# Optimization experiments

Hardware: AMD Instinct MI355X
Metric: run time of the kernel (lower is better)

Reference implementation:

```python
import jax, jax.numpy as jnp
import numpy as np
import math

HEADS = 16
D_MODEL = 1024
D_K = D_MODEL // HEADS


def setup_inputs() -> dict:
    key = jax.random.key(0)
    ks = jax.random.split(key, 11)
    B, S = 2, 2048
    s = 1.0 / math.sqrt(D_MODEL)
    return {
        "q": jax.random.normal(ks[0], (B, S, D_MODEL), jnp.float32),
        "k": jax.random.normal(ks[1], (B, S, D_MODEL), jnp.float32),
        "v": jax.random.normal(ks[2], (B, S, D_MODEL), jnp.float32),
        "Wq": jax.random.normal(ks[3], (D_MODEL, D_MODEL), jnp.float32) * s,
        "bq": jax.random.normal(ks[4], (D_MODEL,), jnp.float32) * s,
        "Wk": jax.random.normal(ks[5], (D_MODEL, D_MODEL), jnp.float32) * s,
        "bk": jax.random.normal(ks[6], (D_MODEL,), jnp.float32) * s,
        "Wv": jax.random.normal(ks[7], (D_MODEL, D_MODEL), jnp.float32) * s,
        "bv": jax.random.normal(ks[8], (D_MODEL,), jnp.float32) * s,
        "Wo": jax.random.normal(ks[9], (D_MODEL, D_MODEL), jnp.float32) * s,
        "bo": jax.random.normal(ks[10], (D_MODEL,), jnp.float32) * s,
    }


def reference(q, k, v, Wq, bq, Wk, bk, Wv, bv, Wo, bo):
    B, S, _ = q.shape
    # linear projections, split heads: [B, H, S, d_k]
    def proj(x, W, b):
        y = x @ W.T + b
        return y.reshape(B, -1, HEADS, D_K).transpose(0, 2, 1, 3)
    qh, kh, vh = proj(q, Wq, bq), proj(k, Wk, bk), proj(v, Wv, bv)
    # abs-modified scaled dot-product attention (no mask, eval -> no dropout)
    scores = jnp.abs(jnp.einsum("bhsd,bhtd->bhst", qh, kh) / math.sqrt(D_K))
    attn = jax.nn.softmax(scores, axis=-1)
    out = jnp.einsum("bhst,bhtd->bhsd", attn, vh)
    concat = out.transpose(0, 2, 1, 3).reshape(B, S, D_MODEL)
    return concat @ Wo.T + bo
```

## Files before the change

kernel.cpp:

```cpp
#include <hip/hip_runtime.h>
#include <hip/hip_bf16.h>

#define HEADS 16
#define DK 64
#define DM 1024
#define SEQ 2048
#define BATCH 2

using bf16x8 = __attribute__((ext_vector_type(8))) short;
using short4v = __attribute__((ext_vector_type(4))) short;
using f32x4 = __attribute__((ext_vector_type(4))) float;

static __device__ __forceinline__ short f2bf(float x) {
  union { float f; unsigned u; } c;
  c.f = x;
  unsigned r = (c.u + 0x7FFFu + ((c.u >> 16) & 1u)) >> 16;
  return (short)r;
}

static __device__ __forceinline__ unsigned pk2bf(float lo, float hi) {
  union { __hip_bfloat162 h; unsigned u; } c;
  c.h = __float22bfloat162_rn(float2{lo, hi});
  return c.u;
}

static __device__ __forceinline__ void gload_lds16(const void* g, void* l) {
  __builtin_amdgcn_global_load_lds(
      (const __attribute__((address_space(1))) void*)g,
      (__attribute__((address_space(3))) void*)l, 16, 0, 0);
}

__global__ __launch_bounds__(256) void cvt7(
    const float* __restrict__ s0, const float* __restrict__ s1,
    const float* __restrict__ s2, const float* __restrict__ s3,
    const float* __restrict__ s4, const float* __restrict__ s5,
    const float* __restrict__ s6, short* d0, short* d1, short* d2, short* d3,
    short* d4, short* d5, short* d6) {
  const int y = blockIdx.y;
  const float* s;
  short* d;
  int n;
  switch (y) {
    case 0: s = s0; d = d0; n = BATCH * SEQ * DM; break;
    case 1: s = s1; d = d1; n = BATCH * SEQ * DM; break;
    case 2: s = s2; d = d2; n = BATCH * SEQ * DM; break;
    case 3: s = s3; d = d3; n = DM * DM; break;
    case 4: s = s4; d = d4; n = DM * DM; break;
    case 5: s = s5; d = d5; n = DM * DM; break;
    default: s = s6; d = d6; n = DM * DM; break;
  }
  const int n4 = n >> 2;
  const int stride = gridDim.x * 256;
  for (int i = blockIdx.x * 256 + threadIdx.x; i < n4; i += stride) {
    float4 v = ((const float4*)s)[i];
    short4v o;
    o.x = f2bf(v.x);
    o.y = f2bf(v.y);
    o.z = f2bf(v.z);
    o.w = f2bf(v.w);
    ((short4v*)d)[i] = o;
  }
}

__global__ __launch_bounds__(256) void proj_qkv(
    const short* __restrict__ Aq, const short* __restrict__ Ak,
    const short* __restrict__ Av, const short* __restrict__ Wq_,
    const short* __restrict__ Wk_, const short* __restrict__ Wv_,
    const float* __restrict__ bq, const float* __restrict__ bk,
    const float* __restrict__ bv, short* __restrict__ Qh,
    short* __restrict__ Kh, short* __restrict__ Vt) {
  __shared__ short smem[128 * 136];
  short* As = smem;
  short* Ws = smem + 8192;

  const int z = blockIdx.z;
  const short* A = z == 0 ? Aq : z == 1 ? Ak : Av;
  const short* W = z == 0 ? Wq_ : z == 1 ? Wk_ : Wv_;
  const float* bias = z == 0 ? bq : z == 1 ? bk : bv;
  short* C = z == 0 ? Qh : z == 1 ? Kh : Vt;
  const bool tr = (z == 2);

  const int tid = threadIdx.x;
  const int wave = tid >> 6, lane = tid & 63;
  const int quad = lane >> 4, l15 = lane & 15;
  const int n0 = blockIdx.x * 128, m0 = blockIdx.y * 128;
  const int mh = (wave & 1) * 64, nh = (wave >> 1) * 64;
  const int ldr = lane >> 3, ldc = lane & 7;

  f32x4 acc[4][4] = {};

  for (int k0 = 0; k0 < 1024; k0 += 64) {
    __syncthreads();
#pragma unroll
    for (int i = 0; i < 8; ++i) {
      int seg = wave * 8 + i;
      int r = (seg & 15) * 8 + ldr;
      int kb = ldc ^ (r & 7);
      if (seg < 16)
        gload_lds16(&A[(size_t)(m0 + r) * 1024 + k0 + kb * 8], &As[seg * 512]);
      else
        gload_lds16(&W[(size_t)(n0 + r) * 1024 + k0 + kb * 8],
                    &Ws[(seg - 16) * 512]);
    }
    __syncthreads();
#pragma unroll
    for (int ks = 0; ks < 2; ++ks) {
      bf16x8 a[4], b[4];
      int kb = ks * 4 + quad;
#pragma unroll
      for (int f = 0; f < 4; ++f) {
        int rm = mh + f * 16 + l15;
        int rn = nh + f * 16 + l15;
        a[f] = *(const bf16x8*)&As[rm * 64 + (kb ^ (rm & 7)) * 8];
        b[f] = *(const bf16x8*)&Ws[rn * 64 + (kb ^ (rn & 7)) * 8];
      }
#pragma unroll
      for (int mf = 0; mf < 4; ++mf)
#pragma unroll
        for (int nf = 0; nf < 4; ++nf)
          acc[mf][nf] = __builtin_amdgcn_mfma_f32_16x16x32_bf16(
              a[mf], b[nf], acc[mf][nf], 0, 0, 0);
    }
  }

  float bvv[4];
#pragma unroll
  for (int nf = 0; nf < 4; ++nf) bvv[nf] = bias[n0 + nh + nf * 16 + l15];

  __syncthreads();
  short* Cb = smem;

  if (!tr) {
    const float osc = (z == 0) ? 0.18033688011112042f : 1.0f;
#pragma unroll
    for (int mf = 0; mf < 4; ++mf)
#pragma unroll
      for (int nf = 0; nf < 4; ++nf)
#pragma unroll
        for (int r = 0; r < 4; ++r)
          Cb[(mh + mf * 16 + quad * 4 + r) * 136 + nh + nf * 16 + l15] =
              f2bf((acc[mf][nf][r] + bvv[nf]) * osc);
    __syncthreads();
#pragma unroll
    for (int j = 0; j < 8; ++j) {
      int cid = tid + 256 * j;
      int row = cid >> 4, cb = cid & 15;
      bf16x8 v = *(const bf16x8*)&Cb[row * 136 + cb * 8];
      int m = m0 + row, n = n0 + cb * 8;
      int b = m >> 11, s = m & (SEQ - 1), h = n >> 6, d = n & 63;
      *(bf16x8*)&C[((size_t)(b * HEADS + h) * SEQ + s) * DK + d] = v;
    }
  } else {
#pragma unroll
    for (int mf = 0; mf < 4; ++mf)
#pragma unroll
      for (int nf = 0; nf < 4; ++nf) {
        short4v p;
        p.x = f2bf(acc[mf][nf][0] + bvv[nf]);
        p.y = f2bf(acc[mf][nf][1] + bvv[nf]);
        p.z = f2bf(acc[mf][nf][2] + bvv[nf]);
        p.w = f2bf(acc[mf][nf][3] + bvv[nf]);
        *(short4v*)&Cb[(nh + nf * 16 + l15) * 136 + mh + mf * 16 + quad * 4] =
            p;
      }
    __syncthreads();
#pragma unroll
    for (int j = 0; j < 8; ++j) {
      int cid = tid + 256 * j;
      int row = cid >> 4, cb = cid & 15;
      bf16x8 v = *(const bf16x8*)&Cb[row * 136 + cb * 8];
      int n = n0 + row, m = m0 + cb * 8;
      int b = m >> 11, s = m & (SEQ - 1), h = n >> 6, d = n & 63;
      *(bf16x8*)&C[((size_t)(b * HEADS + h) * DK + d) * SEQ + s] = v;
    }
  }
}

__global__ __launch_bounds__(256) void proj_out(const short* __restrict__ A,
                                                const short* __restrict__ W,
                                                const float* __restrict__ bias,
                                                float* __restrict__ C) {
  __shared__ short smem[128 * 136];
  short* As = smem;
  short* Ws = smem + 8192;

  const int tid = threadIdx.x;
  const int wave = tid >> 6, lane = tid & 63;
  const int quad = lane >> 4, l15 = lane & 15;
  const int n0 = blockIdx.x * 128, m0 = blockIdx.y * 128;
  const int mh = (wave & 1) * 64, nh = (wave >> 1) * 64;
  const int ldr = lane >> 3, ldc = lane & 7;

  f32x4 acc[4][4] = {};

  for (int k0 = 0; k0 < 1024; k0 += 64) {
    __syncthreads();
#pragma unroll
    for (int i = 0; i < 8; ++i) {
      int seg = wave * 8 + i;
      int r = (seg & 15) * 8 + ldr;
      int kb = ldc ^ (r & 7);
      if (seg < 16)
        gload_lds16(&A[(size_t)(m0 + r) * 1024 + k0 + kb * 8], &As[seg * 512]);
      else
        gload_lds16(&W[(size_t)(n0 + r) * 1024 + k0 + kb * 8],
                    &Ws[(seg - 16) * 512]);
    }
    __syncthreads();
#pragma unroll
    for (int ks = 0; ks < 2; ++ks) {
      bf16x8 a[4], b[4];
      int kb = ks * 4 + quad;
#pragma unroll
      for (int f = 0; f < 4; ++f) {
        int rm = mh + f * 16 + l15;
        int rn = nh + f * 16 + l15;
        a[f] = *(const bf16x8*)&As[rm * 64 + (kb ^ (rm & 7)) * 8];
        b[f] = *(const bf16x8*)&Ws[rn * 64 + (kb ^ (rn & 7)) * 8];
      }
#pragma unroll
      for (int mf = 0; mf < 4; ++mf)
#pragma unroll
        for (int nf = 0; nf < 4; ++nf)
          acc[mf][nf] = __builtin_amdgcn_mfma_f32_16x16x32_bf16(
              a[mf], b[nf], acc[mf][nf], 0, 0, 0);
    }
  }

  float bvv[4];
#pragma unroll
  for (int nf = 0; nf < 4; ++nf) bvv[nf] = bias[n0 + nh + nf * 16 + l15];
#pragma unroll
  for (int mf = 0; mf < 4; ++mf)
#pragma unroll
    for (int nf = 0; nf < 4; ++nf)
#pragma unroll
      for (int r = 0; r < 4; ++r)
        C[(size_t)(m0 + mh + mf * 16 + quad * 4 + r) * 1024 + n0 + nh +
          nf * 16 + l15] = acc[mf][nf][r] + bvv[nf];
}

__global__ __launch_bounds__(256) void attn_mfma(const short* __restrict__ Qh,
                                                 const short* __restrict__ Kh,
                                                 const short* __restrict__ VtG,
                                                 short* __restrict__ concat) {
  __shared__ short Ksm[2][64 * 64];
  __shared__ short Vsm[2][64 * 64];

  const int tid = threadIdx.x;
  const int wave = tid >> 6, lane = tid & 63;
  const int quad = lane >> 4, l15 = lane & 15;
  const int bh = blockIdx.y;
  const int q0 = blockIdx.x * 128;
  const size_t base = (size_t)bh * SEQ * DK;
  const int ldr = lane >> 3, ldc = lane & 7;
  const int NT = SEQ / 64;

  bf16x8 qf[2][2];
#pragma unroll
  for (int mf = 0; mf < 2; ++mf)
#pragma unroll
    for (int ks = 0; ks < 2; ++ks)
      qf[mf][ks] =
          *(const bf16x8*)&Qh[base +
                              (size_t)(q0 + wave * 32 + mf * 16 + l15) * 64 +
                              ks * 32 + quad * 8];

  bf16x8 ones;
#pragma unroll
  for (int i = 0; i < 8; ++i) ones[i] = (short)0x3F80;

  f32x4 O[2][4] = {};
  f32x4 Lacc[2] = {};

  int krow[4];
#pragma unroll
  for (int kf = 0; kf < 4; ++kf)
    krow[kf] = 32 * (kf >> 1) + 8 * (l15 >> 2) + 4 * (kf & 1) + (l15 & 3);

  auto stage = [&](int kt, int buf) {
#pragma unroll
    for (int i = 0; i < 2; ++i) {
      int seg = wave * 2 + i;
      int r = seg * 8 + ldr;
      int kswz = (r & 7) ^ (((r >> 3) & 3) << 1);
      gload_lds16(&Kh[base + (size_t)(kt * 64 + r) * 64 + (ldc ^ kswz) * 8],
                  &Ksm[buf][seg * 512]);
      gload_lds16(&VtG[base + (size_t)r * SEQ + kt * 64 + (ldc ^ (r & 7)) * 8],
                  &Vsm[buf][seg * 512]);
    }
  };

  stage(0, 0);
  __syncthreads();

  int cur = 0;
  for (int kt = 0; kt < NT; ++kt) {
    if (kt + 1 < NT) stage(kt + 1, cur ^ 1);

    const short* Ks = Ksm[cur];
    const short* Vs = Vsm[cur];

    f32x4 sf[2][4] = {};
#pragma unroll
    for (int ks = 0; ks < 2; ++ks) {
      bf16x8 kfr[4];
      int kb = ks * 4 + quad;
#pragma unroll
      for (int kf = 0; kf < 4; ++kf) {
        int n = krow[kf];
        int kswz = (n & 7) ^ (((n >> 3) & 3) << 1);
        kfr[kf] = *(const bf16x8*)&Ks[n * 64 + ((kb ^ kswz) << 3)];
      }
      __builtin_amdgcn_s_setprio(1);
#pragma unroll
      for (int kf = 0; kf < 4; ++kf)
#pragma unroll
        for (int mf = 0; mf < 2; ++mf)
          sf[mf][kf] = __builtin_amdgcn_mfma_f32_16x16x32_bf16(
              kfr[kf], qf[mf][ks], sf[mf][kf], 0, 0, 0);
      __builtin_amdgcn_s_setprio(0);
    }

    bf16x8 pa[2][2];
#pragma unroll
    for (int mf = 0; mf < 2; ++mf)
#pragma unroll
      for (int ks = 0; ks < 2; ++ks) {
        float e[8];
#pragma unroll
        for (int half = 0; half < 2; ++half)
#pragma unroll
          for (int r = 0; r < 4; ++r)
            e[half * 4 + r] =
                __builtin_amdgcn_exp2f(fabsf(sf[mf][2 * ks + half][r]));
        union { unsigned u[4]; bf16x8 v; } t;
        t.u[0] = pk2bf(e[0], e[1]);
        t.u[1] = pk2bf(e[2], e[3]);
        t.u[2] = pk2bf(e[4], e[5]);
        t.u[3] = pk2bf(e[6], e[7]);
        pa[mf][ks] = t.v;
      }

#pragma unroll
    for (int ks = 0; ks < 2; ++ks) {
      int kb = ks * 4 + quad;
      bf16x8 bvf[4];
#pragma unroll
      for (int nf = 0; nf < 4; ++nf) {
        int d = nf * 16 + l15;
        bvf[nf] = *(const bf16x8*)&Vs[d * 64 + ((kb ^ (d & 7)) << 3)];
      }
      __builtin_amdgcn_s_setprio(1);
#pragma unroll
      for (int mf = 0; mf < 2; ++mf) {
#pragma unroll
        for (int nf = 0; nf < 4; ++nf)
          O[mf][nf] = __builtin_amdgcn_mfma_f32_16x16x32_bf16(
              pa[mf][ks], bvf[nf], O[mf][nf], 0, 0, 0);
        Lacc[mf] = __builtin_amdgcn_mfma_f32_16x16x32_bf16(pa[mf][ks], ones,
                                                           Lacc[mf], 0, 0, 0);
      }
      __builtin_amdgcn_s_setprio(0);
    }

    __syncthreads();
    cur ^= 1;
  }

  float inv_[2][4];
#pragma unroll
  for (int mf = 0; mf < 2; ++mf)
#pragma unroll
    for (int r = 0; r < 4; ++r) inv_[mf][r] = 1.f / Lacc[mf][r];

  short* Es = (short*)Ksm;
#pragma unroll
  for (int mf = 0; mf < 2; ++mf)
#pragma unroll
    for (int nf = 0; nf < 4; ++nf)
#pragma unroll
      for (int r = 0; r < 4; ++r) {
        int rw = wave * 32 + mf * 16 + quad * 4 + r;
        int d = nf * 16 + l15;
        Es[rw * 64 + (((d >> 3) ^ (rw & 7)) << 3) + (d & 7)] =
            f2bf(O[mf][nf][r] * inv_[mf][r]);
      }
  __syncthreads();
  const int b = bh >> 4, h = bh & 15;
#pragma unroll
  for (int j = 0; j < 4; ++j) {
    int cid = tid + 256 * j;
    int rw = cid >> 3, g = cid & 7;
    bf16x8 v = *(const bf16x8*)&Es[rw * 64 + ((g ^ (rw & 7)) << 3)];
    *(bf16x8*)&concat[((size_t)(b * SEQ + q0 + rw)) * DM + h * 64 + g * 8] = v;
  }
}

extern "C" void kernel_launch(void* const* d_in, const int* in_sizes, int n_in,
                              void* d_out, int out_size, void* d_ws,
                              size_t ws_size, hipStream_t stream) {
  const float* q = (const float*)d_in[0];
  const float* k = (const float*)d_in[1];
  const float* v = (const float*)d_in[2];
  const float* Wq = (const float*)d_in[3];
  const float* bq = (const float*)d_in[4];
  const float* Wk = (const float*)d_in[5];
  const float* bk = (const float*)d_in[6];
  const float* Wv = (const float*)d_in[7];
  const float* bv = (const float*)d_in[8];
  const float* Wo = (const float*)d_in[9];
  const float* bo = (const float*)d_in[10];

  short* ws = (short*)d_ws;
  const size_t T4 = (size_t)BATCH * SEQ * DM;
  const size_t T1 = (size_t)DM * DM;
  short* qb = ws;
  short* kb_ = ws + T4;
  short* vb = ws + 2 * T4;
  short* Wqb = ws + 3 * T4;
  short* Wkb = Wqb + T1;
  short* Wvb = Wqb + 2 * T1;
  short* Wob = Wqb + 3 * T1;
  short* Qh = Wqb + 4 * T1;
  short* Kh = Qh + T4;
  short* VtG = Qh + 2 * T4;
  short* cc = Qh + 3 * T4;

  cvt7<<<dim3(1024, 7), 256, 0, stream>>>(q, k, v, Wq, Wk, Wv, Wo, qb, kb_, vb,
                                          Wqb, Wkb, Wvb, Wob);

  proj_qkv<<<dim3(DM / 128, (BATCH * SEQ) / 128, 3), 256, 0, stream>>>(
      qb, kb_, vb, Wqb, Wkb, Wvb, bq, bk, bv, Qh, Kh, VtG);

  attn_mfma<<<dim3(SEQ / 128, BATCH * HEADS), 256, 0, stream>>>(Qh, Kh, VtG,
                                                                cc);

  proj_out<<<dim3(DM / 128, (BATCH * SEQ) / 128), 256, 0, stream>>>(
      cc, Wob, bo, (float*)d_out);
}
```

Before: 237.5 us.

## Split attention key tiles across two wave groups with LDS reduction

Doubles the attention block to 512 threads. Two groups of four waves each handle half of every 64-key tile for the same 128 query rows, and their partial O and row-sum accumulators are combined through shared memory at the end. The goal is more waves per block for latency hiding, with half the per-wave work in the inner loop. The cost is a final LDS reduction with extra barriers, duplicated Q fragments across the two groups, and lower per-wave MFMA density.

```diff
diff --git a/kernel.cpp b/kernel.cpp
--- a/kernel.cpp
+++ b/kernel.cpp
@@ -240,16 +240,19 @@
           nf * 16 + l15] = acc[mf][nf][r] + bvv[nf];
 }
 
-__global__ __launch_bounds__(256) void attn_mfma(const short* __restrict__ Qh,
-                                                 const short* __restrict__ Kh,
-                                                 const short* __restrict__ VtG,
-                                                 short* __restrict__ concat) {
-  __shared__ short Ksm[2][64 * 64];
-  __shared__ short Vsm[2][64 * 64];
+__global__ __launch_bounds__(512, 4) void attn_mfma(
+    const short* __restrict__ Qh, const short* __restrict__ Kh,
+    const short* __restrict__ VtG, short* __restrict__ concat) {
+  __shared__ __align__(16) short smem[4 * 64 * 64];
+  __shared__ float Lsm[128];
+  short* Kbuf = smem;
+  short* Vbuf = smem + 2 * 4096;
 
   const int tid = threadIdx.x;
   const int wave = tid >> 6, lane = tid & 63;
   const int quad = lane >> 4, l15 = lane & 15;
+  const int wq = wave & 3;
+  const int wg = wave >> 2;
   const int bh = blockIdx.y;
   const int q0 = blockIdx.x * 128;
   const size_t base = (size_t)bh * SEQ * DK;
@@ -263,7 +266,7 @@
     for (int ks = 0; ks < 2; ++ks)
       qf[mf][ks] =
           *(const bf16x8*)&Qh[base +
-                              (size_t)(q0 + wave * 32 + mf * 16 + l15) * 64 +
+                              (size_t)(q0 + wq * 32 + mf * 16 + l15) * 64 +
                               ks * 32 + quad * 8];
 
   bf16x8 ones;
@@ -273,22 +276,18 @@
   f32x4 O[2][4] = {};
   f32x4 Lacc[2] = {};
 
-  int krow[4];
-#pragma unroll
-  for (int kf = 0; kf < 4; ++kf)
-    krow[kf] = 32 * (kf >> 1) + 8 * (l15 >> 2) + 4 * (kf & 1) + (l15 & 3);
+  int krow[2];
+#pragma unroll
+  for (int kfl = 0; kfl < 2; ++kfl)
+    krow[kfl] = 32 * wg + 8 * (l15 >> 2) + 4 * kfl + (l15 & 3);
 
   auto stage = [&](int kt, int buf) {
-#pragma unroll
-    for (int i = 0; i < 2; ++i) {
-      int seg = wave * 2 + i;
-      int r = seg * 8 + ldr;
-      int kswz = (r & 7) ^ (((r >> 3) & 3) << 1);
-      gload_lds16(&Kh[base + (size_t)(kt * 64 + r) * 64 + (ldc ^ kswz) * 8],
-                  &Ksm[buf][seg * 512]);
-      gload_lds16(&VtG[base + (size_t)r * SEQ + kt * 64 + (ldc ^ (r & 7)) * 8],
-                  &Vsm[buf][seg * 512]);
-    }
+    int r = wave * 8 + ldr;
+    int kswz = (r & 7) ^ (((r >> 3) & 3) << 1);
+    gload_lds16(&Kh[base + (size_t)(kt * 64 + r) * 64 + (ldc ^ kswz) * 8],
+                &Kbuf[buf * 4096 + wave * 512]);
+    gload_lds16(&VtG[base + (size_t)r * SEQ + kt * 64 + (ldc ^ (r & 7)) * 8],
+                &Vbuf[buf * 4096 + wave * 512]);
   };
 
   stage(0, 0);
@@ -298,58 +297,54 @@
   for (int kt = 0; kt < NT; ++kt) {
     if (kt + 1 < NT) stage(kt + 1, cur ^ 1);
 
-    const short* Ks = Ksm[cur];
-    const short* Vs = Vsm[cur];
-
-    f32x4 sf[2][4] = {};
+    const short* Ks = &Kbuf[cur * 4096];
+    const short* Vs = &Vbuf[cur * 4096];
+
+    f32x4 sf[2][2] = {};
 #pragma unroll
     for (int ks = 0; ks < 2; ++ks) {
-      bf16x8 kfr[4];
+      bf16x8 kfr[2];
       int kb = ks * 4 + quad;
 #pragma unroll
-      for (int kf = 0; kf < 4; ++kf) {
-        int n = krow[kf];
+      for (int kfl = 0; kfl < 2; ++kfl) {
+        int n = krow[kfl];
         int kswz = (n & 7) ^ (((n >> 3) & 3) << 1);
-        kfr[kf] = *(const bf16x8*)&Ks[n * 64 + ((kb ^ kswz) << 3)];
+        kfr[kfl] = *(const bf16x8*)&Ks[n * 64 + ((kb ^ kswz) << 3)];
       }
       __builtin_amdgcn_s_setprio(1);
 #pragma unroll
-      for (int kf = 0; kf < 4; ++kf)
+      for (int kfl = 0; kfl < 2; ++kfl)
 #pragma unroll
         for (int mf = 0; mf < 2; ++mf)
-          sf[mf][kf] = __builtin_amdgcn_mfma_f32_16x16x32_bf16(
-              kfr[kf], qf[mf][ks], sf[mf][kf], 0, 0, 0);
+          sf[mf][kfl] = __builtin_amdgcn_mfma_f32_16x16x32_bf16(
+              kfr[kfl], qf[mf][ks], sf[mf][kfl], 0, 0, 0);
       __builtin_amdgcn_s_setprio(0);
     }
 
-    bf16x8 pa[2][2];
-#pragma unroll
-    for (int mf = 0; mf < 2; ++mf)
-#pragma unroll
-      for (int ks = 0; ks < 2; ++ks) {
-        float e[8];
-#pragma unroll
-        for (int half = 0; half < 2; ++half)
-#pragma unroll
-          for (int r = 0; r < 4; ++r)
-            e[half * 4 + r] =
-                __builtin_amdgcn_exp2f(fabsf(sf[mf][2 * ks + half][r]));
-        union { unsigned u[4]; bf16x8 v; } t;
-        t.u[0] = pk2bf(e[0], e[1]);
-        t.u[1] = pk2bf(e[2], e[3]);
-        t.u[2] = pk2bf(e[4], e[5]);
-        t.u[3] = pk2bf(e[6], e[7]);
-        pa[mf][ks] = t.v;
-      }
-
-#pragma unroll
-    for (int ks = 0; ks < 2; ++ks) {
-      int kb = ks * 4 + quad;
+    bf16x8 pa[2];
+#pragma unroll
+    for (int mf = 0; mf < 2; ++mf) {
+      float e[8];
+#pragma unroll
+      for (int kfl = 0; kfl < 2; ++kfl)
+#pragma unroll
+        for (int r = 0; r < 4; ++r)
+          e[kfl * 4 + r] = __builtin_amdgcn_exp2f(fabsf(sf[mf][kfl][r]));
+      union { unsigned u[4]; bf16x8 v; } t;
+      t.u[0] = pk2bf(e[0], e[1]);
+      t.u[1] = pk2bf(e[2], e[3]);
+      t.u[2] = pk2bf(e[4], e[5]);
+      t.u[3] = pk2bf(e[6], e[7]);
+      pa[mf] = t.v;
+    }
+
+    {
+      int gb = wg * 4 + quad;
       bf16x8 bvf[4];
 #pragma unroll
       for (int nf = 0; nf < 4; ++nf) {
         int d = nf * 16 + l15;
-        bvf[nf] = *(const bf16x8*)&Vs[d * 64 + ((kb ^ (d & 7)) << 3)];
+        bvf[nf] = *(const bf16x8*)&Vs[d * 64 + ((gb ^ (d & 7)) << 3)];
       }
       __builtin_amdgcn_s_setprio(1);
 #pragma unroll
@@ -357,8 +352,8 @@
 #pragma unroll
         for (int nf = 0; nf < 4; ++nf)
           O[mf][nf] = __builtin_amdgcn_mfma_f32_16x16x32_bf16(
-              pa[mf][ks], bvf[nf], O[mf][nf], 0, 0, 0);
-        Lacc[mf] = __builtin_amdgcn_mfma_f32_16x16x32_bf16(pa[mf][ks], ones,
+              pa[mf], bvf[nf], O[mf][nf], 0, 0, 0);
+        Lacc[mf] = __builtin_amdgcn_mfma_f32_16x16x32_bf16(pa[mf], ones,
                                                            Lacc[mf], 0, 0, 0);
       }
       __builtin_amdgcn_s_setprio(0);
@@ -368,29 +363,63 @@
     cur ^= 1;
   }
 
+  float* Osm = (float*)smem;
+  if (wg == 1) {
+#pragma unroll
+    for (int mf = 0; mf < 2; ++mf)
+#pragma unroll
+      for (int nf = 0; nf < 4; ++nf) {
+        int d = nf * 16 + l15;
+        int rowb = (wq * 32 + mf * 16 + quad * 4) ^ ((d & 7) << 2);
+        *(f32x4*)&Osm[d * 128 + rowb] = O[mf][nf];
+      }
+    if (l15 == 0)
+#pragma unroll
+      for (int mf = 0; mf < 2; ++mf)
+#pragma unroll
+        for (int r = 0; r < 4; ++r)
+          Lsm[wq * 32 + mf * 16 + quad * 4 + r] = Lacc[mf][r];
+  }
+  __syncthreads();
+
   float inv_[2][4];
-#pragma unroll
-  for (int mf = 0; mf < 2; ++mf)
-#pragma unroll
-    for (int r = 0; r < 4; ++r) inv_[mf][r] = 1.f / Lacc[mf][r];
-
-  short* Es = (short*)Ksm;
-#pragma unroll
-  for (int mf = 0; mf < 2; ++mf)
-#pragma unroll
-    for (int nf = 0; nf < 4; ++nf)
-#pragma unroll
-      for (int r = 0; r < 4; ++r) {
-        int rw = wave * 32 + mf * 16 + quad * 4 + r;
+  if (wg == 0) {
+#pragma unroll
+    for (int mf = 0; mf < 2; ++mf)
+#pragma unroll
+      for (int nf = 0; nf < 4; ++nf) {
         int d = nf * 16 + l15;
-        Es[rw * 64 + (((d >> 3) ^ (rw & 7)) << 3) + (d & 7)] =
-            f2bf(O[mf][nf][r] * inv_[mf][r]);
-      }
+        int rowb = (wq * 32 + mf * 16 + quad * 4) ^ ((d & 7) << 2);
+        O[mf][nf] += *(const f32x4*)&Osm[d * 128 + rowb];
+      }
+#pragma unroll
+    for (int mf = 0; mf < 2; ++mf)
+#pragma unroll
+      for (int r = 0; r < 4; ++r)
+        inv_[mf][r] =
+            1.f / (Lacc[mf][r] + Lsm[wq * 32 + mf * 16 + quad * 4 + r]);
+  }
+  __syncthreads();
+
+  short* Es = smem;
+  if (wg == 0) {
+#pragma unroll
+    for (int mf = 0; mf < 2; ++mf)
+#pragma unroll
+      for (int nf = 0; nf < 4; ++nf)
+#pragma unroll
+        for (int r = 0; r < 4; ++r) {
+          int rw = wq * 32 + mf * 16 + quad * 4 + r;
+          int d = nf * 16 + l15;
+          Es[rw * 64 + (((d >> 3) ^ (rw & 7)) << 3) + (d & 7)] =
+              f2bf(O[mf][nf][r] * inv_[mf][r]);
+        }
+  }
   __syncthreads();
   const int b = bh >> 4, h = bh & 15;
 #pragma unroll
-  for (int j = 0; j < 4; ++j) {
-    int cid = tid + 256 * j;
+  for (int j = 0; j < 2; ++j) {
+    int cid = tid + 512 * j;
     int rw = cid >> 3, g = cid & 7;
     bf16x8 v = *(const bf16x8*)&Es[rw * 64 + ((g ^ (rw & 7)) << 3)];
     *(bf16x8*)&concat[((size_t)(b * SEQ + q0 + rw)) * DM + h * 64 + g * 8] = v;
@@ -433,7 +462,7 @@
   proj_qkv<<<dim3(DM / 128, (BATCH * SEQ) / 128, 3), 256, 0, stream>>>(
       qb, kb_, vb, Wqb, Wkb, Wvb, bq, bk, bv, Qh, Kh, VtG);
 
-  attn_mfma<<<dim3(SEQ / 128, BATCH * HEADS), 256, 0, stream>>>(Qh, Kh, VtG,
+  attn_mfma<<<dim3(SEQ / 128, BATCH * HEADS), 512, 0, stream>>>(Qh, Kh, VtG,
                                                                 cc);
 
   proj_out<<<dim3(DM / 128, (BATCH * SEQ) / 128), 256, 0, stream>>>(
```

Measured after the change: 225.2 us. 5.2% less time.
